# Kernel tuning notes

Measured on AMD Instinct MI355X. Metric: run time of the kernel, lower is better.

The kernel has to match this reference:

```python
import jax, jax.numpy as jnp
import numpy as np

H = 512   # hidden_dim (args.hidden_dim)
D = 128   # data_dim (tones)
N = 64    # num_sequences
T = 512   # max_length


def setup_inputs() -> dict:
    key = jax.random.key(0)
    k1, k2, k3, k4 = jax.random.split(key, 4)
    # Transition matrix: rows on the simplex, biased toward identity (Dirichlet(0.9*I + 0.1) prior).
    probs_x = jax.nn.softmax(jax.random.normal(k1, (H, H)) + 2.0 * jnp.eye(H), axis=-1)
    # Bernoulli emission probabilities (Beta(0.1, 0.9) prior -> values in (0,1), skewed low).
    probs_y = jax.nn.sigmoid(jax.random.normal(k2, (H, D)) - 1.0)
    # Observed binary tone sequences.
    sequences = (jax.random.uniform(k3, (N, T, D)) < 0.3).astype(jnp.float32)
    # Valid lengths in [T//2, T].
    lengths = jnp.sort(jax.random.randint(k4, (N,), T // 2, T + 1)).astype(jnp.int32)
    return {"sequences": sequences, "lengths": lengths, "probs_x": probs_x, "probs_y": probs_y}


def reference(sequences, lengths, probs_x, probs_y):
    """Enumerated-HMM forward algorithm: log p(sequences[n, :lengths[n]]) per sequence.

    Matches Pyro's parallel enumeration of x_t ~ Categorical(probs_x[x_{t-1}]) starting
    from x = 0, with observations y_t ~ Bernoulli(probs_y[x_t]) masked by t < lengths.
    """
    N_, T_, D_ = sequences.shape
    log_px = jnp.log(probs_x)        # [H, H]
    log_py = jnp.log(probs_y)        # [H, D]
    log_1mpy = jnp.log1p(-probs_y)   # [H, D]

    # Bernoulli emission log-likelihood summed over the tones plate: [N, T, H]
    emit = (jnp.einsum('ntd,hd->nth', sequences, log_py)
            + jnp.einsum('ntd,hd->nth', 1.0 - sequences, log_1mpy))

    # t = 0: initial hidden state drawn from probs_x[0] (x starts at 0).
    log_alpha0 = log_px[0][None, :] + emit[:, 0]   # [N, H] (lengths >= 1 so t=0 is unmasked)

    emits = jnp.moveaxis(emit[:, 1:], 1, 0)        # [T-1, N, H]
    ts = jnp.arange(1, T_)

    def step(log_alpha, inp):
        emit_t, t = inp
        # logsumexp over previous state: [N, H_prev] + [H_prev, H_next] -> [N, H_next]
        new = jax.nn.logsumexp(log_alpha[:, :, None] + log_px[None, :, :], axis=1) + emit_t
        mask = (t < lengths)[:, None]
        return jnp.where(mask, new, log_alpha), None

    log_alpha, _ = jax.lax.scan(step, log_alpha0, (emits, ts))
    return jax.nn.logsumexp(log_alpha, axis=-1)    # [N] per-sequence log-likelihood
```

## Files before the change

### kernel.cpp

```cpp
#include <hip/hip_runtime.h>
#include <stdint.h>

#define Hn 512
#define Dn 128
#define Nn 64
#define Tn 512
#define NT (Nn*Tn)

typedef unsigned int uint;
typedef unsigned short ushort;
typedef unsigned long long u64;

typedef __attribute__((ext_vector_type(4))) float f32x4;
typedef __attribute__((ext_vector_type(8))) int i32x8;
typedef __attribute__((ext_vector_type(8))) short short8;

#define WG_BARRIER() asm volatile("s_waitcnt lgkmcnt(0)\n\ts_barrier" ::: "memory")


__device__ inline float bf2f(ushort u) { union { uint i; float f; } v; v.i = uint(u) << 16; return v.f; }
__device__ inline float ubits(uint u) { union { uint i; float f; } v; v.i = u; return v.f; }
__device__ inline ushort f2bf(float f) {
  union { uint i; float f; } v; v.f = f;
  uint u = v.i;
  uint r = (u + 0x7FFFu + ((u >> 16) & 1u)) >> 16;
  return ushort(r);
}
__device__ inline float fp8val(uint b) {
  uint e = (b >> 3) & 15u, m = b & 7u;
  return e ? ldexpf((float)(8u + m), (int)e - 10) : ldexpf((float)m, -9);
}
__device__ inline u64 pack8fp8(const float* v, float qs) {
  int lo = 0, hi = 0;
  lo = __builtin_amdgcn_cvt_pk_fp8_f32(v[0] * qs, v[1] * qs, lo, false);
  lo = __builtin_amdgcn_cvt_pk_fp8_f32(v[2] * qs, v[3] * qs, lo, true);
  hi = __builtin_amdgcn_cvt_pk_fp8_f32(v[4] * qs, v[5] * qs, hi, false);
  hi = __builtin_amdgcn_cvt_pk_fp8_f32(v[6] * qs, v[7] * qs, hi, true);
  return (u64)(uint)lo | ((u64)(uint)hi << 32);
}
__device__ inline int permcol(int c) {
  return (c & ~63) | ((c & 12) << 2) | ((c & 48) >> 2) | (c & 3);
}

__global__ void k_prep(const float* __restrict__ py, ushort* __restrict__ wmatb,
                       float* __restrict__ bias) {
  int h = blockIdx.x, d = threadIdx.x;
  float p = py[h * Dn + d];
  float lp = logf(p), l1 = log1pf(-p);
  wmatb[h * Dn + d] = f2bf(lp - l1);
  float v = l1;
  for (int o = 1; o < 64; o <<= 1) v += __shfl_xor(v, o, 64);
  __shared__ float s2[2];
  if ((threadIdx.x & 63) == 0) s2[threadIdx.x >> 6] = v;
  __syncthreads();
  if (threadIdx.x == 0) bias[h] = s2[0] + s2[1];
}

__global__ __launch_bounds__(256) void k_pq(const float* __restrict__ px,
                                            float* __restrict__ rcsg, float* __restrict__ px0sp,
                                            u64* __restrict__ pq) {
  __shared__ float ksl[512][17];
  __shared__ float pm[16][17];
  __shared__ float csL[16];
  int ntg = blockIdx.x;
  int t = threadIdx.x;
  for (int i = 0; i < 8; i++) {
    int q = i * 256 + t;
    int row = q >> 2, c4 = q & 3;
    float4 v = *(const float4*)(px + (size_t)row * Hn + ntg * 16 + c4 * 4);
    ksl[row][c4 * 4 + 0] = v.x; ksl[row][c4 * 4 + 1] = v.y;
    ksl[row][c4 * 4 + 2] = v.z; ksl[row][c4 * 4 + 3] = v.w;
  }
  __syncthreads();
  {
    int c = t & 15, ch = t >> 4;
    float m = 0.f;
#pragma unroll
    for (int r = 0; r < 32; r++) m = fmaxf(m, ksl[ch * 32 + r][c]);
    pm[ch][c] = m;
  }
  __syncthreads();
  if (t < 16) {
    float m = pm[0][t];
#pragma unroll
    for (int i = 1; i < 16; i++) m = fmaxf(m, pm[i][t]);
    float c = 448.0f / m;
    csL[t] = c;
    rcsg[ntg * 16 + t] = m * (1.0f / 448.0f);
    px0sp[permcol(ntg * 16 + t)] = px[ntg * 16 + t] * c;
  }
  __syncthreads();
  int kb = t >> 6, lane = t & 63, qa = lane >> 4, c15 = lane & 15;
  float csv = csL[c15];
  int kbase = kb * 128 + (qa >> 1) * 64 + (qa & 1) * 8;
  size_t base = ((size_t)(((ntg >> 2) * 16 + kb * 4 + (ntg & 3)) * 64 + lane)) * 4;
#pragma unroll
  for (int d = 0; d < 4; d++) {
    float vv[8];
#pragma unroll
    for (int b = 0; b < 8; b++) {
      int jj = d * 8 + b;
      int kk = kbase + (((jj >> 2) & 3) << 4) + ((jj >> 4) << 2) + (jj & 3);
      vv[b] = ksl[kk][c15];
    }
    pq[base + d] = pack8fp8(vv, csv);
  }
}

__global__ __launch_bounds__(256, 2) void k_emit3(
    const float* __restrict__ A, const ushort* __restrict__ wmatb,
    const float* __restrict__ bias, const float* __restrict__ rcsg,
    ushort* __restrict__ eb, float* __restrict__ rm) {
  __shared__ ushort Bs[128][136];
  __shared__ ushort As[64][136];
  __shared__ float biasL[512];
  __shared__ float rcsL[512];
  int t = threadIdx.x;
  int r0 = blockIdx.x * 64;
  for (int i = 0; i < 8; i++) {
    int q = i * 256 + t, row = q >> 5, c4 = q & 31;
    float4 v = *(const float4*)(A + (size_t)(r0 + row) * Dn + c4 * 4);
    ushort4 u4 = {f2bf(v.x), f2bf(v.y), f2bf(v.z), f2bf(v.w)};
    *(ushort4*)&As[row][c4 * 4] = u4;
  }
  biasL[t] = bias[t]; biasL[t + 256] = bias[t + 256];
  rcsL[t] = rcsg[t];  rcsL[t + 256] = rcsg[t + 256];
  __syncthreads();

  const int w = t >> 6, lane = t & 63, l15 = lane & 15, g4 = lane >> 4;
  short8 afr[4];
#pragma unroll
  for (int kt = 0; kt < 4; kt++)
    afr[kt] = *(const short8*)&As[w * 16 + l15][kt * 32 + g4 * 8];

  f32x4 acc[32];
  for (int cc = 0; cc < 4; cc++) {
    __syncthreads();
    for (int i = 0; i < 8; i++) {
      int q = i * 256 + t, row = q >> 4, c = q & 15;
      *(uint4*)&Bs[row][c * 8] = *(const uint4*)(wmatb + (cc * 128 + row) * 128 + c * 8);
    }
    __syncthreads();
#pragma unroll
    for (int n8 = 0; n8 < 8; n8++) {
      int nt = cc * 8 + n8;
      f32x4 a = {0.f, 0.f, 0.f, 0.f};
#pragma unroll
      for (int kt = 0; kt < 4; kt++) {
        short8 bfr = *(const short8*)&Bs[n8 * 16 + l15][kt * 32 + g4 * 8];
        a = __builtin_amdgcn_mfma_f32_16x16x32_bf16(afr[kt], bfr, a, 0, 0, 0);
      }
      acc[nt] = a;
    }
  }
  float mrow[4] = {-1e30f, -1e30f, -1e30f, -1e30f};
#pragma unroll
  for (int nt = 0; nt < 32; nt++) {
    float bv = biasL[nt * 16 + l15];
#pragma unroll
    for (int r = 0; r < 4; r++) {
      float v = acc[nt][r] + bv;
      acc[nt][r] = v;
      mrow[r] = fmaxf(mrow[r], v);
    }
  }
#pragma unroll
  for (int o = 1; o < 16; o <<= 1) {
    mrow[0] = fmaxf(mrow[0], __shfl_xor(mrow[0], o, 64));
    mrow[1] = fmaxf(mrow[1], __shfl_xor(mrow[1], o, 64));
    mrow[2] = fmaxf(mrow[2], __shfl_xor(mrow[2], o, 64));
    mrow[3] = fmaxf(mrow[3], __shfl_xor(mrow[3], o, 64));
  }
  if (l15 == 0) {
#pragma unroll
    for (int r = 0; r < 4; r++) rm[(size_t)(r0 + w * 16 + g4 * 4 + r)] = mrow[r];
  }
  ushort* ebase = eb + (size_t)(r0 + w * 16 + g4 * 4) * Hn;
#pragma unroll
  for (int nt = 0; nt < 32; nt++) {
    int colp = (nt >> 2) * 64 + (l15 >> 2) * 16 + (nt & 3) * 4 + (l15 & 3);
    float rc = rcsL[nt * 16 + l15];
#pragma unroll
    for (int r = 0; r < 4; r++) {
      float e = __expf(acc[nt][r] - mrow[r]) * rc;
      ebase[(size_t)r * Hn + colp] = f2bf(e);
    }
  }
}

__global__ __launch_bounds__(512, 2) void k_rec9(
    const ushort* __restrict__ eb, const float* __restrict__ rm,
    const u64* __restrict__ pq, const float* __restrict__ px0sp,
    const int* __restrict__ lens, float* __restrict__ outp) {
  const int grp = blockIdx.x;
  const int t = threadIdx.x;
  const int w = t >> 6;
  const int lane = t & 63, qg = lane >> 4, l15 = lane & 15;

  __shared__ uint4 BfI[32][16];
  __shared__ float sredM[16][12];
  __shared__ float rmsL[16];
  __shared__ int lenl[16];

  i32x8 PRv[16];
  {
    const uint4* pqv = (const uint4*)pq;
#pragma unroll
    for (int f = 0; f < 16; f++) {
      uint4 p0 = pqv[((size_t)(w * 16 + f) * 64 + lane) * 2 + 0];
      uint4 p1 = pqv[((size_t)(w * 16 + f) * 64 + lane) * 2 + 1];
      i32x8 v = {(int)p0.x, (int)p0.y, (int)p0.z, (int)p0.w,
                 (int)p1.x, (int)p1.y, (int)p1.z, (int)p1.w};
      PRv[f] = v;
    }
  }

  if (t < 16) lenl[t] = lens[grp * 16 + t];
  const size_t seqstride = (size_t)Tn * Hn;
  const ushort* myrow = eb + (size_t)(grp * 16 + l15) * seqstride + w * 64 + qg * 16;
  uint4* myslot = &BfI[w * 4 + qg][l15];

  float4 uv0, uv1, uv2, uv3;
  {
    uint4 e0 = *(const uint4*)myrow;
    uint4 e1 = *(const uint4*)(myrow + 8);
    float4 p0 = *(const float4*)(px0sp + w * 64 + qg * 16 + 0);
    float4 p1 = *(const float4*)(px0sp + w * 64 + qg * 16 + 4);
    float4 p2 = *(const float4*)(px0sp + w * 64 + qg * 16 + 8);
    float4 p3 = *(const float4*)(px0sp + w * 64 + qg * 16 + 12);
    uv0.x = p0.x * ubits(e0.x << 16);  uv0.y = p0.y * ubits(e0.x & 0xffff0000u);
    uv0.z = p0.z * ubits(e0.y << 16);  uv0.w = p0.w * ubits(e0.y & 0xffff0000u);
    uv1.x = p1.x * ubits(e0.z << 16);  uv1.y = p1.y * ubits(e0.z & 0xffff0000u);
    uv1.z = p1.z * ubits(e0.w << 16);  uv1.w = p1.w * ubits(e0.w & 0xffff0000u);
    uv2.x = p2.x * ubits(e1.x << 16);  uv2.y = p2.y * ubits(e1.x & 0xffff0000u);
    uv2.z = p2.z * ubits(e1.y << 16);  uv2.w = p2.w * ubits(e1.y & 0xffff0000u);
    uv3.x = p3.x * ubits(e1.z << 16);  uv3.y = p3.y * ubits(e1.z & 0xffff0000u);
    uv3.z = p3.z * ubits(e1.w << 16);  uv3.w = p3.w * ubits(e1.w & 0xffff0000u);
    float m01 = fmaxf(fmaxf(fmaxf(uv0.x, uv0.y), fmaxf(uv0.z, uv0.w)),
                      fmaxf(fmaxf(uv1.x, uv1.y), fmaxf(uv1.z, uv1.w)));
    float m23 = fmaxf(fmaxf(fmaxf(uv2.x, uv2.y), fmaxf(uv2.z, uv2.w)),
                      fmaxf(fmaxf(uv3.x, uv3.y), fmaxf(uv3.z, uv3.w)));
    float mxv = fmaxf(m01, m23);
    mxv = fmaxf(mxv, __shfl_xor(mxv, 16, 64));
    mxv = fmaxf(mxv, __shfl_xor(mxv, 32, 64));
    if (qg == 0) sredM[l15][w] = mxv;
  }
  WG_BARRIER();
  const int t_end = lenl[15];
  const int lenq = lenl[l15];
  float L2acc;
  u64 myf0, myf1;

  {
    float4 g0 = *(const float4*)&sredM[l15][0];
    float4 g1 = *(const float4*)&sredM[l15][4];
    float gm = fmaxf(fmaxf(fmaxf(g0.x, g0.y), fmaxf(g0.z, g0.w)),
                     fmaxf(fmaxf(g1.x, g1.y), fmaxf(g1.z, g1.w)));
    L2acc = __log2f(gm);
    float qs = 448.0f * __builtin_amdgcn_rcpf(gm);
    float v0[8] = {uv0.x, uv0.y, uv0.z, uv0.w, uv1.x, uv1.y, uv1.z, uv1.w};
    float v1[8] = {uv2.x, uv2.y, uv2.z, uv2.w, uv3.x, uv3.y, uv3.z, uv3.w};
    myf0 = pack8fp8(v0, qs);
    myf1 = pack8fp8(v1, qs);
    *myslot = (uint4){(uint)myf0, (uint)(myf0 >> 32), (uint)myf1, (uint)(myf1 >> 32)};
  }

  const ushort* epp = myrow + Hn;
  uint4 bpA = *(const uint4*)epp;
  uint4 bpB = *(const uint4*)(epp + 8);
  epp += Hn;

  for (int ts = 1; ts < t_end; ts++) {
    WG_BARRIER();

    f32x4 ac0 = {0.f, 0.f, 0.f, 0.f}, ac1 = {0.f, 0.f, 0.f, 0.f};
    f32x4 ac2 = {0.f, 0.f, 0.f, 0.f}, ac3 = {0.f, 0.f, 0.f, 0.f};
    __builtin_amdgcn_s_setprio(1);
#pragma unroll
    for (int kb = 0; kb < 4; kb++) {
      uint4 b0 = BfI[kb * 8 + qg * 2 + 0][l15];
      uint4 b1 = BfI[kb * 8 + qg * 2 + 1][l15];
      i32x8 bf = {(int)b0.x, (int)b0.y, (int)b0.z, (int)b0.w,
                  (int)b1.x, (int)b1.y, (int)b1.z, (int)b1.w};
      ac0 = __builtin_amdgcn_mfma_scale_f32_16x16x128_f8f6f4(
          PRv[kb * 4 + 0], bf, ac0, 0, 0, 0, 0x7F7F7F7F, 0, 0x7F7F7F7F);
      ac1 = __builtin_amdgcn_mfma_scale_f32_16x16x128_f8f6f4(
          PRv[kb * 4 + 1], bf, ac1, 0, 0, 0, 0x7F7F7F7F, 0, 0x7F7F7F7F);
      ac2 = __builtin_amdgcn_mfma_scale_f32_16x16x128_f8f6f4(
          PRv[kb * 4 + 2], bf, ac2, 0, 0, 0, 0x7F7F7F7F, 0, 0x7F7F7F7F);
      ac3 = __builtin_amdgcn_mfma_scale_f32_16x16x128_f8f6f4(
          PRv[kb * 4 + 3], bf, ac3, 0, 0, 0, 0x7F7F7F7F, 0, 0x7F7F7F7F);
    }
    __builtin_amdgcn_s_setprio(0);

    uint4 bqA = *(const uint4*)epp;
    uint4 bqB = *(const uint4*)(epp + 8);
    epp += Hn;

    {
      uv0.x = ac0[0] * ubits(bpA.x << 16);  uv0.y = ac0[1] * ubits(bpA.x & 0xffff0000u);
      uv0.z = ac0[2] * ubits(bpA.y << 16);  uv0.w = ac0[3] * ubits(bpA.y & 0xffff0000u);
      uv1.x = ac1[0] * ubits(bpA.z << 16);  uv1.y = ac1[1] * ubits(bpA.z & 0xffff0000u);
      uv1.z = ac1[2] * ubits(bpA.w << 16);  uv1.w = ac1[3] * ubits(bpA.w & 0xffff0000u);
      uv2.x = ac2[0] * ubits(bpB.x << 16);  uv2.y = ac2[1] * ubits(bpB.x & 0xffff0000u);
      uv2.z = ac2[2] * ubits(bpB.y << 16);  uv2.w = ac2[3] * ubits(bpB.y & 0xffff0000u);
      uv3.x = ac3[0] * ubits(bpB.z << 16);  uv3.y = ac3[1] * ubits(bpB.z & 0xffff0000u);
      uv3.z = ac3[2] * ubits(bpB.w << 16);  uv3.w = ac3[3] * ubits(bpB.w & 0xffff0000u);
      float m01 = fmaxf(fmaxf(fmaxf(uv0.x, uv0.y), fmaxf(uv0.z, uv0.w)),
                        fmaxf(fmaxf(uv1.x, uv1.y), fmaxf(uv1.z, uv1.w)));
      float m23 = fmaxf(fmaxf(fmaxf(uv2.x, uv2.y), fmaxf(uv2.z, uv2.w)),
                        fmaxf(fmaxf(uv3.x, uv3.y), fmaxf(uv3.z, uv3.w)));
      float mxv = fmaxf(m01, m23);
      mxv = fmaxf(mxv, __shfl_xor(mxv, 16, 64));
      mxv = fmaxf(mxv, __shfl_xor(mxv, 32, 64));
      if (qg == 0) sredM[l15][w] = mxv;
    }
    WG_BARRIER();

    if (ts < lenq) {
      float4 g0 = *(const float4*)&sredM[l15][0];
      float4 g1 = *(const float4*)&sredM[l15][4];
      float gm = fmaxf(fmaxf(fmaxf(g0.x, g0.y), fmaxf(g0.z, g0.w)),
                       fmaxf(fmaxf(g1.x, g1.y), fmaxf(g1.z, g1.w)));
      L2acc += __log2f(gm);
      float qs = 448.0f * __builtin_amdgcn_rcpf(gm);
      float v0[8] = {uv0.x, uv0.y, uv0.z, uv0.w, uv1.x, uv1.y, uv1.z, uv1.w};
      float v1[8] = {uv2.x, uv2.y, uv2.z, uv2.w, uv3.x, uv3.y, uv3.z, uv3.w};
      myf0 = pack8fp8(v0, qs);
      myf1 = pack8fp8(v1, qs);
      *myslot = (uint4){(uint)myf0, (uint)(myf0 >> 32), (uint)myf1, (uint)(myf1 >> 32)};
    }
    bpA = bqA; bpB = bqB;
  }

  WG_BARRIER();
  {
    float ps = 0.f;
#pragma unroll
    for (int j = 0; j < 8; j++) {
      ps += fp8val((uint)(myf0 >> (8 * j)) & 0xffu);
      ps += fp8val((uint)(myf1 >> (8 * j)) & 0xffu);
    }
    ps += __shfl_xor(ps, 16, 64);
    ps += __shfl_xor(ps, 32, 64);
    if (qg == 0) sredM[l15][w] = ps;
  }
  {
    int sq = 2 * w + (lane >> 5), tl = lane & 31;
    const float* rp = rm + (size_t)(grp * 16 + sq) * Tn;
    int ls = lenl[sq];
    float rs = 0.f;
#pragma unroll
    for (int k = 0; k < 16; k++) {
      int idx = tl + 32 * k;
      float v = rp[idx];
      rs += (idx < ls) ? v : 0.f;
    }
#pragma unroll
    for (int o = 1; o < 32; o <<= 1) rs += __shfl_xor(rs, o, 64);
    if ((lane & 31) == 0) rmsL[sq] = rs;
  }
  __syncthreads();
  if (t < 16) {
    float4 s0 = *(const float4*)&sredM[t][0];
    float4 s1 = *(const float4*)&sredM[t][4];
    float Ss = (s0.x + s0.y) + (s0.z + s0.w) + (s1.x + s1.y) + (s1.z + s1.w);
    outp[grp * 16 + t] = 0.6931471805599453f * L2acc - (float)lenq * 6.104793232414985f
                         + logf(Ss) + rmsL[t];
  }
}

extern "C" void kernel_launch(void* const* d_in, const int* in_sizes, int n_in,
                              void* d_out, int out_size, void* d_ws, size_t ws_size,
                              hipStream_t stream) {
  const float* seq = (const float*)d_in[0];
  const int* lens = (const int*)d_in[1];
  const float* px = (const float*)d_in[2];
  const float* py = (const float*)d_in[3];
  char* ws = (char*)d_ws;
  ushort* emitb = (ushort*)(ws + 0x0000000);
  float* rm     = (float*)(ws + 0x2000000);
  ushort* wmatb = (ushort*)(ws + 0x2020000);
  float* bias   = (float*)(ws + 0x2060000);
  float* rcsg   = (float*)(ws + 0x2062000);
  float* px0sp  = (float*)(ws + 0x2063000);
  u64* pq       = (u64*)(ws + 0x2070000);
  float* outp   = (float*)d_out;

  hipLaunchKernelGGL(k_prep, dim3(512), dim3(128), 0, stream, py, wmatb, bias);
  hipLaunchKernelGGL(k_pq, dim3(32), dim3(256), 0, stream, px, rcsg, px0sp, pq);
  hipLaunchKernelGGL(k_emit3, dim3(NT / 64), dim3(256), 0, stream, seq, wmatb, bias, rcsg, emitb, rm);
  hipLaunchKernelGGL(k_rec9, dim3(4), dim3(512), 0, stream, emitb, rm, pq, px0sp, lens, outp);
}
```

Baseline: 606.5 us.

## Merge prep kernels, hoist B-fragment LDS loads, use three-input max reductions

Fuses the py-preparation and px-quantisation kernels into one launch, with block index selecting the role, which removes one kernel launch and its gap. In the recurrence loop, all eight B-fragment LDS reads are issued before the MFMA chain rather than interleaved with it, so LDS latency can overlap. Max reductions are restructured around a three-operand helper so the compiler can emit v_max3 instructions. The hoisted loads raise register pressure in the serial recurrence kernel.

```diff
diff --git a/kernel.cpp b/kernel.cpp
--- a/kernel.cpp
+++ b/kernel.cpp
@@ -16,6 +16,8 @@
 typedef __attribute__((ext_vector_type(8))) short short8;
 
 #define WG_BARRIER() asm volatile("s_waitcnt lgkmcnt(0)\n\ts_barrier" ::: "memory")
+
+__device__ inline float max3f(float a, float b, float c) { return fmaxf(fmaxf(a, b), c); }
 
 
 __device__ inline float bf2f(ushort u) { union { uint i; float f; } v; v.i = uint(u) << 16; return v.f; }
@@ -42,28 +44,29 @@
   return (c & ~63) | ((c & 12) << 2) | ((c & 48) >> 2) | (c & 3);
 }
 
-__global__ void k_prep(const float* __restrict__ py, ushort* __restrict__ wmatb,
-                       float* __restrict__ bias) {
-  int h = blockIdx.x, d = threadIdx.x;
-  float p = py[h * Dn + d];
-  float lp = logf(p), l1 = log1pf(-p);
-  wmatb[h * Dn + d] = f2bf(lp - l1);
-  float v = l1;
-  for (int o = 1; o < 64; o <<= 1) v += __shfl_xor(v, o, 64);
-  __shared__ float s2[2];
-  if ((threadIdx.x & 63) == 0) s2[threadIdx.x >> 6] = v;
-  __syncthreads();
-  if (threadIdx.x == 0) bias[h] = s2[0] + s2[1];
-}
-
-__global__ __launch_bounds__(256) void k_pq(const float* __restrict__ px,
-                                            float* __restrict__ rcsg, float* __restrict__ px0sp,
-                                            u64* __restrict__ pq) {
+__global__ __launch_bounds__(256) void k_preppq(
+    const float* __restrict__ py, const float* __restrict__ px,
+    ushort* __restrict__ wmatb, float* __restrict__ bias,
+    float* __restrict__ rcsg, float* __restrict__ px0sp, u64* __restrict__ pq) {
   __shared__ float ksl[512][17];
   __shared__ float pm[16][17];
   __shared__ float csL[16];
-  int ntg = blockIdx.x;
+  __shared__ float s2[4];
+  int b = blockIdx.x;
   int t = threadIdx.x;
+  if (b < 256) {
+    int h = 2 * b + (t >> 7), d = t & 127;
+    float p = py[h * Dn + d];
+    float lp = logf(p), l1 = log1pf(-p);
+    wmatb[h * Dn + d] = f2bf(lp - l1);
+    float v = l1;
+    for (int o = 1; o < 64; o <<= 1) v += __shfl_xor(v, o, 64);
+    if ((t & 63) == 0) s2[t >> 6] = v;
+    __syncthreads();
+    if ((t & 127) == 0) bias[h] = s2[(t >> 7) * 2] + s2[(t >> 7) * 2 + 1];
+    return;
+  }
+  int ntg = b - 256;
   for (int i = 0; i < 8; i++) {
     int q = i * 256 + t;
     int row = q >> 2, c4 = q & 3;
@@ -76,14 +79,16 @@
     int c = t & 15, ch = t >> 4;
     float m = 0.f;
 #pragma unroll
-    for (int r = 0; r < 32; r++) m = fmaxf(m, ksl[ch * 32 + r][c]);
+    for (int r = 0; r < 30; r += 3) m = max3f(m, fmaxf(ksl[ch * 32 + r][c], ksl[ch * 32 + r + 1][c]), ksl[ch * 32 + r + 2][c]);
+    m = max3f(m, ksl[ch * 32 + 30][c], ksl[ch * 32 + 31][c]);
     pm[ch][c] = m;
   }
   __syncthreads();
   if (t < 16) {
     float m = pm[0][t];
 #pragma unroll
-    for (int i = 1; i < 16; i++) m = fmaxf(m, pm[i][t]);
+    for (int i = 1; i < 15; i += 2) m = max3f(m, pm[i][t], pm[i + 1][t]);
+    m = fmaxf(m, pm[15][t]);
     float c = 448.0f / m;
     csL[t] = c;
     rcsg[ntg * 16 + t] = m * (1.0f / 448.0f);
@@ -98,10 +103,10 @@
   for (int d = 0; d < 4; d++) {
     float vv[8];
 #pragma unroll
-    for (int b = 0; b < 8; b++) {
-      int jj = d * 8 + b;
+    for (int bb = 0; bb < 8; bb++) {
+      int jj = d * 8 + bb;
       int kk = kbase + (((jj >> 2) & 3) << 4) + ((jj >> 4) << 2) + (jj & 3);
-      vv[b] = ksl[kk][c15];
+      vv[bb] = ksl[kk][c15];
     }
     pq[base + d] = pack8fp8(vv, csv);
   }
@@ -236,11 +241,10 @@
     uv2.z = p2.z * ubits(e1.y << 16);  uv2.w = p2.w * ubits(e1.y & 0xffff0000u);
     uv3.x = p3.x * ubits(e1.z << 16);  uv3.y = p3.y * ubits(e1.z & 0xffff0000u);
     uv3.z = p3.z * ubits(e1.w << 16);  uv3.w = p3.w * ubits(e1.w & 0xffff0000u);
-    float m01 = fmaxf(fmaxf(fmaxf(uv0.x, uv0.y), fmaxf(uv0.z, uv0.w)),
-                      fmaxf(fmaxf(uv1.x, uv1.y), fmaxf(uv1.z, uv1.w)));
-    float m23 = fmaxf(fmaxf(fmaxf(uv2.x, uv2.y), fmaxf(uv2.z, uv2.w)),
-                      fmaxf(fmaxf(uv3.x, uv3.y), fmaxf(uv3.z, uv3.w)));
-    float mxv = fmaxf(m01, m23);
+    float ma = max3f(max3f(uv0.x, uv0.y, uv0.z), max3f(uv0.w, uv1.x, uv1.y),
+                     max3f(uv1.z, uv1.w, uv2.x));
+    float mb = max3f(max3f(uv2.y, uv2.z, uv2.w), max3f(uv3.x, uv3.y, uv3.z), uv3.w);
+    float mxv = fmaxf(ma, mb);
     mxv = fmaxf(mxv, __shfl_xor(mxv, 16, 64));
     mxv = fmaxf(mxv, __shfl_xor(mxv, 32, 64));
     if (qg == 0) sredM[l15][w] = mxv;
@@ -254,8 +258,7 @@
   {
     float4 g0 = *(const float4*)&sredM[l15][0];
     float4 g1 = *(const float4*)&sredM[l15][4];
-    float gm = fmaxf(fmaxf(fmaxf(g0.x, g0.y), fmaxf(g0.z, g0.w)),
-                     fmaxf(fmaxf(g1.x, g1.y), fmaxf(g1.z, g1.w)));
+    float gm = fmaxf(max3f(max3f(g0.x, g0.y, g0.z), max3f(g0.w, g1.x, g1.y), g1.z), g1.w);
     L2acc = __log2f(gm);
     float qs = 448.0f * __builtin_amdgcn_rcpf(gm);
     float v0[8] = {uv0.x, uv0.y, uv0.z, uv0.w, uv1.x, uv1.y, uv1.z, uv1.w};
@@ -273,13 +276,17 @@
   for (int ts = 1; ts < t_end; ts++) {
     WG_BARRIER();
 
+    uint4 bfr[8];
+#pragma unroll
+    for (int s = 0; s < 8; s++) bfr[s] = BfI[(s >> 1) * 8 + qg * 2 + (s & 1)][l15];
+
     f32x4 ac0 = {0.f, 0.f, 0.f, 0.f}, ac1 = {0.f, 0.f, 0.f, 0.f};
     f32x4 ac2 = {0.f, 0.f, 0.f, 0.f}, ac3 = {0.f, 0.f, 0.f, 0.f};
     __builtin_amdgcn_s_setprio(1);
 #pragma unroll
     for (int kb = 0; kb < 4; kb++) {
-      uint4 b0 = BfI[kb * 8 + qg * 2 + 0][l15];
-      uint4 b1 = BfI[kb * 8 + qg * 2 + 1][l15];
+      uint4 b0 = bfr[kb * 2 + 0];
+      uint4 b1 = bfr[kb * 2 + 1];
       i32x8 bf = {(int)b0.x, (int)b0.y, (int)b0.z, (int)b0.w,
                   (int)b1.x, (int)b1.y, (int)b1.z, (int)b1.w};
       ac0 = __builtin_amdgcn_mfma_scale_f32_16x16x128_f8f6f4(
@@ -306,11 +313,10 @@
       uv2.z = ac2[2] * ubits(bpB.y << 16);  uv2.w = ac2[3] * ubits(bpB.y & 0xffff0000u);
       uv3.x = ac3[0] * ubits(bpB.z << 16);  uv3.y = ac3[1] * ubits(bpB.z & 0xffff0000u);
       uv3.z = ac3[2] * ubits(bpB.w << 16);  uv3.w = ac3[3] * ubits(bpB.w & 0xffff0000u);
-      float m01 = fmaxf(fmaxf(fmaxf(uv0.x, uv0.y), fmaxf(uv0.z, uv0.w)),
-                        fmaxf(fmaxf(uv1.x, uv1.y), fmaxf(uv1.z, uv1.w)));
-      float m23 = fmaxf(fmaxf(fmaxf(uv2.x, uv2.y), fmaxf(uv2.z, uv2.w)),
-                        fmaxf(fmaxf(uv3.x, uv3.y), fmaxf(uv3.z, uv3.w)));
-      float mxv = fmaxf(m01, m23);
+      float ma = max3f(max3f(uv0.x, uv0.y, uv0.z), max3f(uv0.w, uv1.x, uv1.y),
+                       max3f(uv1.z, uv1.w, uv2.x));
+      float mb = max3f(max3f(uv2.y, uv2.z, uv2.w), max3f(uv3.x, uv3.y, uv3.z), uv3.w);
+      float mxv = fmaxf(ma, mb);
       mxv = fmaxf(mxv, __shfl_xor(mxv, 16, 64));
       mxv = fmaxf(mxv, __shfl_xor(mxv, 32, 64));
       if (qg == 0) sredM[l15][w] = mxv;
@@ -320,8 +326,7 @@
     if (ts < lenq) {
       float4 g0 = *(const float4*)&sredM[l15][0];
       float4 g1 = *(const float4*)&sredM[l15][4];
-      float gm = fmaxf(fmaxf(fmaxf(g0.x, g0.y), fmaxf(g0.z, g0.w)),
-                       fmaxf(fmaxf(g1.x, g1.y), fmaxf(g1.z, g1.w)));
+      float gm = fmaxf(max3f(max3f(g0.x, g0.y, g0.z), max3f(g0.w, g1.x, g1.y), g1.z), g1.w);
       L2acc += __log2f(gm);
       float qs = 448.0f * __builtin_amdgcn_rcpf(gm);
       float v0[8] = {uv0.x, uv0.y, uv0.z, uv0.w, uv1.x, uv1.y, uv1.z, uv1.w};
@@ -387,8 +392,7 @@
   u64* pq       = (u64*)(ws + 0x2070000);
   float* outp   = (float*)d_out;
 
-  hipLaunchKernelGGL(k_prep, dim3(512), dim3(128), 0, stream, py, wmatb, bias);
-  hipLaunchKernelGGL(k_pq, dim3(32), dim3(256), 0, stream, px, rcsg, px0sp, pq);
+  hipLaunchKernelGGL(k_preppq, dim3(288), dim3(256), 0, stream, py, px, wmatb, bias, rcsg, px0sp, pq);
   hipLaunchKernelGGL(k_emit3, dim3(NT / 64), dim3(256), 0, stream, seq, wmatb, bias, rcsg, emitb, rm);
   hipLaunchKernelGGL(k_rec9, dim3(4), dim3(512), 0, stream, emitb, rm, pq, px0sp, lens, outp);
 }
```

New measurement: 576.7 us (median of 2 runs). -4.9%, faster.
